# Kernel tuning notes

Measured on AMD Instinct MI355X. Metric: run time of the kernel, lower is better.

The kernel has to match this reference:

```python
import jax, jax.numpy as jnp
import numpy as np

B, M, N, D = 2, 2048, 2048, 2048
N_H, D_H, D_R = 16, 128, 64
THETA = 1000000.0
SCALE = 1.0 / np.sqrt(D_H + D_R)


def build_rope_cache(seq_len, dim, theta):
    freqs = 1.0 / theta ** (jnp.arange(0, dim, 2, dtype=jnp.float32) / dim)
    t = jnp.arange(seq_len, dtype=jnp.float32)
    freqs = jnp.outer(t, freqs)  # (S, dim//2)
    cos = jnp.repeat(jnp.cos(freqs), 2, axis=-1)  # (S, dim)
    sin = jnp.repeat(jnp.sin(freqs), 2, axis=-1)
    return cos, sin


def apply_rope(x, cos, sin):
    # x: (..., S, dim); cos/sin broadcastable (S, dim)
    x_rot = jnp.stack([-x[..., 1::2], x[..., ::2]], axis=-1).reshape(x.shape)
    return x * cos + x_rot * sin


def setup_inputs() -> dict:
    key = jax.random.key(0)
    ks = jax.random.split(key, 8)
    std = 0.02
    return {
        "query": jax.random.normal(ks[0], (B, M, D), jnp.float32),
        "key_value": jax.random.normal(ks[1], (B, N, D), jnp.float32),
        "W_QC": jax.random.normal(ks[2], (N_H * D_H, D), jnp.float32) * std,
        "W_KC": jax.random.normal(ks[3], (N_H * D_H, D), jnp.float32) * std,
        "W_QR": jax.random.normal(ks[4], (N_H * D_R, D), jnp.float32) * std,
        "W_KR": jax.random.normal(ks[5], (N_H * D_R, D), jnp.float32) * std,
        "W_V": jax.random.normal(ks[6], (N_H * D_H, D), jnp.float32) * std,
        "W_O": jax.random.normal(ks[7], (D, N_H * D_H), jnp.float32) * std,
    }


def reference(query, key_value, W_QC, W_KC, W_QR, W_KR, W_V, W_O):
    # projections: torch Linear is x @ W.T
    Q_C = (query @ W_QC.T).reshape(B, M, N_H, D_H).transpose(0, 2, 1, 3)  # (B,H,M,dh)
    K_C = (key_value @ W_KC.T).reshape(B, N, N_H, D_H).transpose(0, 2, 1, 3)
    Q_R = (query @ W_QR.T).reshape(B, M, N_H, D_R).transpose(0, 2, 1, 3)  # (B,H,M,dR)
    K_R = (key_value @ W_KR.T).reshape(B, N, N_H, D_R).transpose(0, 2, 1, 3)
    cos, sin = build_rope_cache(max(M, N), D_R, THETA)
    Q_R = apply_rope(Q_R, cos[:M], sin[:M])
    K_R = apply_rope(K_R, cos[:N], sin[:N])
    scores = (jnp.einsum('bhmd,bhnd->bhmn', Q_C, K_C)
              + jnp.einsum('bhmr,bhnr->bhmn', Q_R, K_R)) * SCALE
    attn = jax.nn.softmax(scores, axis=-1)
    V = (key_value @ W_V.T).reshape(B, N, N_H, D_H).transpose(0, 2, 1, 3)
    out = jnp.einsum('bhmn,bhnd->bhmd', attn, V)  # (B,H,M,dh)
    out = out.transpose(0, 2, 1, 3).reshape(B, M, N_H * D_H)
    return out @ W_O.T
```

## Files before the change

### kernel.cpp

```cpp
#include <hip/hip_runtime.h>
#include <hip/hip_bf16.h>

typedef unsigned short u16;
typedef __attribute__((ext_vector_type(8))) short short8;
typedef __attribute__((ext_vector_type(4))) float floatx4;

#define B_SZ 2
#define M_SZ 2048
#define N_SZ 2048
#define SCALE_F 0.07216878364870323f

__device__ __forceinline__ u16 f2b(float f) {
    unsigned int x = __builtin_bit_cast(unsigned int, f);
    unsigned int r = (x + 0x7fffu + ((x >> 16) & 1u)) >> 16;
    return (u16)r;
}
__device__ __forceinline__ float b2f(u16 u) {
    unsigned int x = ((unsigned int)u) << 16;
    return __builtin_bit_cast(float, x);
}
__device__ __forceinline__ void async16(const void* g, void* l) {
    __builtin_amdgcn_global_load_lds(
        (const __attribute__((address_space(1))) void*)g,
        (__attribute__((address_space(3))) void*)l, 16, 0, 0);
}

__global__ void cast_k(const float* __restrict__ s, u16* __restrict__ d, long n)
{
    const long i = ((long)blockIdx.x * 256 + threadIdx.x) * 4;
    if (i >= n) return;
    const float4 v = *(const float4*)(s + i);
    unsigned long long pk = (unsigned long long)f2b(v.x)
                          | ((unsigned long long)f2b(v.y) << 16)
                          | ((unsigned long long)f2b(v.z) << 32)
                          | ((unsigned long long)f2b(v.w) << 48);
    *(unsigned long long*)(d + i) = pk;
}

__global__ void rope_k(u16* __restrict__ buf)
{
    const int idx = blockIdx.x * 256 + threadIdx.x;
    const int row = idx >> 9;
    const int pr  = idx & 511;
    const int j   = pr & 31;
    const int pos = row & 2047;
    const float f   = powf(1.0e6f, -(float)j * (1.0f / 32.0f));
    const float ang = (float)pos * f;
    float sn, cs;
    sincosf(ang, &sn, &cs);
    u16* pp = buf + ((long)row << 10) + (pr << 1);
    const float x0 = b2f(pp[0]);
    const float x1 = b2f(pp[1]);
    pp[0] = f2b(x0 * cs - x1 * sn);
    pp[1] = f2b(x1 * cs + x0 * sn);
}

template<int MODE>
__global__ void __launch_bounds__(256, 2)
gemm_bt(const u16* __restrict__ A, const u16* __restrict__ Bw,
        void* __restrict__ Cout, int K, int Ndim)
{
    __shared__ u16 As[128 * 64];
    __shared__ u16 Bs[128 * 64];
    const int t = threadIdx.x;
    const int w = t >> 6;
    const int lane = t & 63;
    const int lq = lane >> 4, lr = lane & 15;
    const long tileM = (long)blockIdx.x * 128;
    const long tileN = (long)blockIdx.y * 128;
    const int wm = (w >> 1) * 64, wn = (w & 1) * 64;

    const floatx4 fzero = {0.f, 0.f, 0.f, 0.f};
    floatx4 acc[4][4];
#pragma unroll
    for (int i = 0; i < 4; ++i)
#pragma unroll
        for (int j = 0; j < 4; ++j) acc[i][j] = fzero;

    for (int k0 = 0; k0 < K; k0 += 64) {
#pragma unroll
        for (int r = 0; r < 4; ++r) {
            const int c = r * 256 + t;
            const int row = c >> 3, cc = c & 7;
            const int gcol = ((cc ^ (row & 7)) << 3);
            async16(A + (tileM + row) * (long)K + k0 + gcol, (char*)As + c * 16);
        }
#pragma unroll
        for (int r = 0; r < 4; ++r) {
            const int c = r * 256 + t;
            const int row = c >> 3, cc = c & 7;
            const int gcol = ((cc ^ (row & 7)) << 3);
            async16(Bw + (tileN + row) * (long)K + k0 + gcol, (char*)Bs + c * 16);
        }
        __builtin_amdgcn_s_waitcnt(0);
        __syncthreads();
#pragma unroll
        for (int kk = 0; kk < 2; ++kk) {
            short8 af[4], bfr[4];
#pragma unroll
            for (int i = 0; i < 4; ++i) {
                const int row = wm + 16 * i + lr;
                const int cc = (kk * 4 + lq) ^ (row & 7);
                af[i] = *(const short8*)(As + row * 64 + cc * 8);
            }
#pragma unroll
            for (int j = 0; j < 4; ++j) {
                const int row = wn + 16 * j + lr;
                const int cc = (kk * 4 + lq) ^ (row & 7);
                bfr[j] = *(const short8*)(Bs + row * 64 + cc * 8);
            }
#pragma unroll
            for (int i = 0; i < 4; ++i)
#pragma unroll
                for (int j = 0; j < 4; ++j)
                    acc[i][j] = __builtin_amdgcn_mfma_f32_16x16x32_bf16(
                        af[i], bfr[j], acc[i][j], 0, 0, 0);
        }
        __syncthreads();
    }

#pragma unroll
    for (int i = 0; i < 4; ++i) {
#pragma unroll
        for (int j = 0; j < 4; ++j) {
            const long row0 = tileM + wm + 16 * i + 4 * lq;
            const long col  = tileN + wn + 16 * j + lr;
#pragma unroll
            for (int r = 0; r < 4; ++r) {
                const float v = acc[i][j][r];
                const long row = row0 + r;
                if (MODE == 0) {
                    ((u16*)Cout)[row * Ndim + col] = f2b(v);
                } else if (MODE == 1) {
                    const long b = row >> 11, nn = row & 2047;
                    ((u16*)Cout)[((b * 2048 + col) << 11) + nn] = f2b(v);
                } else {
                    ((float*)Cout)[row * Ndim + col] = v;
                }
            }
        }
    }
}

__global__ void __launch_bounds__(256, 2)
flash_attn(const u16* __restrict__ QC, const u16* __restrict__ QR,
           const u16* __restrict__ KC, const u16* __restrict__ KR,
           const u16* __restrict__ VT, u16* __restrict__ Obuf)
{
    __shared__ u16 KC_s[64 * 128];
    __shared__ u16 KR_s[64 * 64];
    __shared__ u16 VT_s[128 * 64];
    __shared__ u16 P_s[4][32 * 72];

    const int t = threadIdx.x;
    const int w = t >> 6;
    const int lane = t & 63;
    const int lq = lane >> 4, lr = lane & 15;
    const int mb = blockIdx.x;
    const int h  = blockIdx.y;
    const int b  = blockIdx.z;
    const int mbase = mb * 128 + w * 32;

    short8 aq[2][6];
#pragma unroll
    for (int i = 0; i < 2; ++i) {
        const long m = mbase + 16 * i + lr;
        const u16* qc = QC + ((long)b * M_SZ + m) * 2048 + h * 128;
        const u16* qr = QR + ((long)b * M_SZ + m) * 1024 + h * 64;
#pragma unroll
        for (int kc = 0; kc < 4; ++kc) aq[i][kc]     = *(const short8*)(qc + kc * 32 + lq * 8);
#pragma unroll
        for (int kc = 0; kc < 2; ++kc) aq[i][4 + kc] = *(const short8*)(qr + kc * 32 + lq * 8);
    }

    const floatx4 fzero = {0.f, 0.f, 0.f, 0.f};
    float mst[2][4], lst[2][4];
    floatx4 oacc[2][8];
#pragma unroll
    for (int i = 0; i < 2; ++i) {
#pragma unroll
        for (int r = 0; r < 4; ++r) { mst[i][r] = -1e30f; lst[i][r] = 0.f; }
#pragma unroll
        for (int jn = 0; jn < 8; ++jn) oacc[i][jn] = fzero;
    }

    const u16* kc_g = KC + ((long)b * N_SZ) * 2048 + h * 128;
    const u16* kr_g = KR + ((long)b * N_SZ) * 1024 + h * 64;
    const u16* vt_g = VT + ((long)(b * 16 + h) * 128) * 2048;

    for (int kt = 0; kt < 32; ++kt) {
#pragma unroll
        for (int r = 0; r < 4; ++r) {
            const int c = r * 256 + t;
            const int krow = c >> 4, cc = c & 15;
            const int gc = cc ^ (krow & 7);
            async16(kc_g + (long)(kt * 64 + krow) * 2048 + gc * 8, (char*)KC_s + c * 16);
        }
#pragma unroll
        for (int r = 0; r < 2; ++r) {
            const int c = r * 256 + t;
            const int krow = c >> 3, cc = c & 7;
            const int gc = cc ^ (krow & 7);
            async16(kr_g + (long)(kt * 64 + krow) * 1024 + gc * 8, (char*)KR_s + c * 16);
        }
#pragma unroll
        for (int r = 0; r < 4; ++r) {
            const int c = r * 256 + t;
            const int drow = c >> 3, cc = c & 7;
            const int gc = cc ^ (drow & 7);
            async16(vt_g + (long)drow * 2048 + kt * 64 + gc * 8, (char*)VT_s + c * 16);
        }
        __builtin_amdgcn_s_waitcnt(0);
        __syncthreads();

        floatx4 s[2][4];
#pragma unroll
        for (int i = 0; i < 2; ++i)
#pragma unroll
            for (int j = 0; j < 4; ++j) s[i][j] = fzero;
#pragma unroll
        for (int kc = 0; kc < 6; ++kc) {
            short8 bfr[4];
#pragma unroll
            for (int j = 0; j < 4; ++j) {
                const int krow = 16 * j + lr;
                if (kc < 4) {
                    const int cc = (4 * kc + lq) ^ (krow & 7);
                    bfr[j] = *(const short8*)(KC_s + krow * 128 + cc * 8);
                } else {
                    const int cc = (4 * (kc - 4) + lq) ^ (krow & 7);
                    bfr[j] = *(const short8*)(KR_s + krow * 64 + cc * 8);
                }
            }
#pragma unroll
            for (int i = 0; i < 2; ++i)
#pragma unroll
                for (int j = 0; j < 4; ++j)
                    s[i][j] = __builtin_amdgcn_mfma_f32_16x16x32_bf16(
                        aq[i][kc], bfr[j], s[i][j], 0, 0, 0);
        }

#pragma unroll
        for (int i = 0; i < 2; ++i) {
            float rmax[4], rsum[4], alpha[4];
#pragma unroll
            for (int j = 0; j < 4; ++j)
#pragma unroll
                for (int r = 0; r < 4; ++r) s[i][j][r] *= SCALE_F;
#pragma unroll
            for (int r = 0; r < 4; ++r)
                rmax[r] = fmaxf(fmaxf(s[i][0][r], s[i][1][r]), fmaxf(s[i][2][r], s[i][3][r]));
#pragma unroll
            for (int d = 1; d < 16; d <<= 1)
#pragma unroll
                for (int r = 0; r < 4; ++r)
                    rmax[r] = fmaxf(rmax[r], __shfl_xor(rmax[r], d, 64));
#pragma unroll
            for (int r = 0; r < 4; ++r) {
                const float mnew = fmaxf(mst[i][r], rmax[r]);
                alpha[r] = __expf(mst[i][r] - mnew);
                mst[i][r] = mnew;
                rsum[r] = 0.f;
            }
#pragma unroll
            for (int j = 0; j < 4; ++j)
#pragma unroll
                for (int r = 0; r < 4; ++r) {
                    const float p = __expf(s[i][j][r] - mst[i][r]);
                    s[i][j][r] = p;
                    rsum[r] += p;
                }
#pragma unroll
            for (int d = 1; d < 16; d <<= 1)
#pragma unroll
                for (int r = 0; r < 4; ++r)
                    rsum[r] += __shfl_xor(rsum[r], d, 64);
#pragma unroll
            for (int r = 0; r < 4; ++r)
                lst[i][r] = lst[i][r] * alpha[r] + rsum[r];
#pragma unroll
            for (int jn = 0; jn < 8; ++jn)
#pragma unroll
                for (int r = 0; r < 4; ++r) oacc[i][jn][r] *= alpha[r];
            u16* pw = &P_s[w][0];
#pragma unroll
            for (int j = 0; j < 4; ++j)
#pragma unroll
                for (int r = 0; r < 4; ++r)
                    pw[(16 * i + 4 * lq + r) * 72 + 16 * j + lr] = f2b(s[i][j][r]);
        }

#pragma unroll
        for (int kc = 0; kc < 2; ++kc) {
            short8 ap[2];
#pragma unroll
            for (int i = 0; i < 2; ++i)
                ap[i] = *(const short8*)(&P_s[w][0] + (16 * i + lr) * 72 + kc * 32 + lq * 8);
#pragma unroll
            for (int jn = 0; jn < 8; ++jn) {
                const int drow = 16 * jn + lr;
                const int cc = (4 * kc + lq) ^ (drow & 7);
                const short8 bv = *(const short8*)(VT_s + drow * 64 + cc * 8);
#pragma unroll
                for (int i = 0; i < 2; ++i)
                    oacc[i][jn] = __builtin_amdgcn_mfma_f32_16x16x32_bf16(
                        ap[i], bv, oacc[i][jn], 0, 0, 0);
            }
        }
        __syncthreads();
    }

#pragma unroll
    for (int i = 0; i < 2; ++i)
#pragma unroll
        for (int jn = 0; jn < 8; ++jn)
#pragma unroll
            for (int r = 0; r < 4; ++r) {
                const long row = mbase + 16 * i + 4 * lq + r;
                const int d = 16 * jn + lr;
                const float v = oacc[i][jn][r] / lst[i][r];
                Obuf[((long)b * M_SZ + row) * 2048 + h * 128 + d] = f2b(v);
            }
}

extern "C" void kernel_launch(void* const* d_in, const int* in_sizes, int n_in,
                              void* d_out, int out_size, void* d_ws, size_t ws_size,
                              hipStream_t stream)
{
    (void)in_sizes; (void)n_in; (void)out_size; (void)ws_size;
    const float* q   = (const float*)d_in[0];
    const float* kv  = (const float*)d_in[1];
    const float* wqc = (const float*)d_in[2];
    const float* wkc = (const float*)d_in[3];
    const float* wqr = (const float*)d_in[4];
    const float* wkr = (const float*)d_in[5];
    const float* wv  = (const float*)d_in[6];
    const float* wo  = (const float*)d_in[7];

    u16* p = (u16*)d_ws;
    u16* qbf  = p; p += 8388608;
    u16* kvbf = p; p += 8388608;
    u16* wqcb = p; p += 4194304;
    u16* wkcb = p; p += 4194304;
    u16* wqrb = p; p += 2097152;
    u16* wkrb = p; p += 2097152;
    u16* wvb  = p; p += 4194304;
    u16* wob  = p; p += 4194304;
    u16* QCb  = p; p += 8388608;
    u16* KCb  = p; p += 8388608;
    u16* QRb  = p; p += 4194304;
    u16* KRb  = p; p += 4194304;
    u16* VTb  = p; p += 8388608;
    u16* Ob   = p; p += 8388608;

    cast_k<<<8192, 256, 0, stream>>>(q,   qbf,  8388608);
    cast_k<<<8192, 256, 0, stream>>>(kv,  kvbf, 8388608);
    cast_k<<<4096, 256, 0, stream>>>(wqc, wqcb, 4194304);
    cast_k<<<4096, 256, 0, stream>>>(wkc, wkcb, 4194304);
    cast_k<<<2048, 256, 0, stream>>>(wqr, wqrb, 2097152);
    cast_k<<<2048, 256, 0, stream>>>(wkr, wkrb, 2097152);
    cast_k<<<4096, 256, 0, stream>>>(wv,  wvb,  4194304);
    cast_k<<<4096, 256, 0, stream>>>(wo,  wob,  4194304);

    dim3 g1(32, 16), g2(32, 8);
    gemm_bt<0><<<g1, 256, 0, stream>>>(qbf,  wqcb, QCb, 2048, 2048);
    gemm_bt<0><<<g1, 256, 0, stream>>>(kvbf, wkcb, KCb, 2048, 2048);
    gemm_bt<0><<<g2, 256, 0, stream>>>(qbf,  wqrb, QRb, 2048, 1024);
    gemm_bt<0><<<g2, 256, 0, stream>>>(kvbf, wkrb, KRb, 2048, 1024);
    gemm_bt<1><<<g1, 256, 0, stream>>>(kvbf, wvb,  VTb, 2048, 2048);

    rope_k<<<8192, 256, 0, stream>>>(QRb);
    rope_k<<<8192, 256, 0, stream>>>(KRb);

    dim3 gf(16, 16, 2);
    flash_attn<<<gf, 256, 0, stream>>>(QCb, QRb, KCb, KRb, VTb, Ob);

    gemm_bt<2><<<g1, 256, 0, stream>>>(Ob, wob, d_out, 2048, 2048);
}
```

Measured before the change: 585.3 us.

## Fuse casts, concatenate projection weights, fuse RoPE into GEMM epilogue, streamline softmax

Replaces the eight cast launches with a single multi-segment cast kernel that also folds the softmax scale and log2(e) into the query. Projection weights are concatenated so Q and KV projections each run as one GEMM, and RoPE and V-transpose are applied in the GEMM epilogue, which removes the separate rope kernels and their memory round-trips. The flash-attention softmax switches to exp2, skips the rescale when no row max increases, and packs P conversions. GEMM launch bounds are raised to 3 blocks per SM, which may constrain registers. Folding the scale into bf16 query rounding slightly changes numerics.

Measured after the change: 513.9 us. -12.2%, faster.

```diff
diff --git a/kernel.cpp b/kernel.cpp
--- a/kernel.cpp
+++ b/kernel.cpp
@@ -2,22 +2,27 @@
 #include <hip/hip_bf16.h>
 
 typedef unsigned short u16;
+typedef unsigned int u32;
+typedef unsigned long long u64;
 typedef __attribute__((ext_vector_type(8))) short short8;
 typedef __attribute__((ext_vector_type(4))) float floatx4;
 
-#define B_SZ 2
-#define M_SZ 2048
-#define N_SZ 2048
-#define SCALE_F 0.07216878364870323f
+#if __has_builtin(__builtin_amdgcn_exp2f)
+#define EXP2F(x) __builtin_amdgcn_exp2f(x)
+#else
+#define EXP2F(x) exp2f(x)
+#endif
+
+#define QSCALE (0.07216878364870323f * 1.4426950408889634f)
+#define ROPE_C 0.62286151779f
 
 __device__ __forceinline__ u16 f2b(float f) {
     unsigned int x = __builtin_bit_cast(unsigned int, f);
     unsigned int r = (x + 0x7fffu + ((x >> 16) & 1u)) >> 16;
     return (u16)r;
 }
-__device__ __forceinline__ float b2f(u16 u) {
-    unsigned int x = ((unsigned int)u) << 16;
-    return __builtin_bit_cast(float, x);
+__device__ __forceinline__ u32 pk2(float a, float b) {
+    return (u32)f2b(a) | ((u32)f2b(b) << 16);
 }
 __device__ __forceinline__ void async16(const void* g, void* l) {
     __builtin_amdgcn_global_load_lds(
@@ -25,40 +30,32 @@
         (__attribute__((address_space(3))) void*)l, 16, 0, 0);
 }
 
-__global__ void cast_k(const float* __restrict__ s, u16* __restrict__ d, long n)
+struct CastArgs {
+    const float* src[8];
+    u16* dst[8];
+    float scale[8];
+    int startblk[8];
+};
+
+__global__ void cast_all_k(CastArgs a)
 {
-    const long i = ((long)blockIdx.x * 256 + threadIdx.x) * 4;
-    if (i >= n) return;
-    const float4 v = *(const float4*)(s + i);
-    unsigned long long pk = (unsigned long long)f2b(v.x)
-                          | ((unsigned long long)f2b(v.y) << 16)
-                          | ((unsigned long long)f2b(v.z) << 32)
-                          | ((unsigned long long)f2b(v.w) << 48);
-    *(unsigned long long*)(d + i) = pk;
-}
-
-__global__ void rope_k(u16* __restrict__ buf)
-{
-    const int idx = blockIdx.x * 256 + threadIdx.x;
-    const int row = idx >> 9;
-    const int pr  = idx & 511;
-    const int j   = pr & 31;
-    const int pos = row & 2047;
-    const float f   = powf(1.0e6f, -(float)j * (1.0f / 32.0f));
-    const float ang = (float)pos * f;
-    float sn, cs;
-    sincosf(ang, &sn, &cs);
-    u16* pp = buf + ((long)row << 10) + (pr << 1);
-    const float x0 = b2f(pp[0]);
-    const float x1 = b2f(pp[1]);
-    pp[0] = f2b(x0 * cs - x1 * sn);
-    pp[1] = f2b(x1 * cs + x0 * sn);
-}
-
-template<int MODE>
-__global__ void __launch_bounds__(256, 2)
+    const int bid = blockIdx.x;
+    int s = 0;
+#pragma unroll
+    for (int i = 1; i < 8; ++i) s += (bid >= a.startblk[i]);
+    const long idx = ((long)(bid - a.startblk[s]) * 256 + threadIdx.x) * 4;
+    const float4 v = *(const float4*)(a.src[s] + idx);
+    const float sc = a.scale[s];
+    const u64 pk = (u64)pk2(v.x * sc, v.y * sc)
+                 | ((u64)pk2(v.z * sc, v.w * sc) << 32);
+    *(u64*)(a.dst[s] + idx) = pk;
+}
+
+template<int EPI>
+__global__ void __launch_bounds__(256, 3)
 gemm_bt(const u16* __restrict__ A, const u16* __restrict__ Bw,
-        void* __restrict__ Cout, int K, int Ndim)
+        void* __restrict__ out0, u16* __restrict__ out1, u16* __restrict__ out2,
+        int K)
 {
     __shared__ u16 As[128 * 64];
     __shared__ u16 Bs[128 * 64];
@@ -119,24 +116,42 @@
         __syncthreads();
     }
 
+    const bool isV    = (EPI == 1) && (tileN >= 3072);
+    const bool isRope = (EPI != 2) && !isV && (tileN >= 2048);
+
 #pragma unroll
     for (int i = 0; i < 4; ++i) {
 #pragma unroll
         for (int j = 0; j < 4; ++j) {
             const long row0 = tileM + wm + 16 * i + 4 * lq;
             const long col  = tileN + wn + 16 * j + lr;
-#pragma unroll
-            for (int r = 0; r < 4; ++r) {
-                const float v = acc[i][j][r];
-                const long row = row0 + r;
-                if (MODE == 0) {
-                    ((u16*)Cout)[row * Ndim + col] = f2b(v);
-                } else if (MODE == 1) {
-                    const long b = row >> 11, nn = row & 2047;
-                    ((u16*)Cout)[((b * 2048 + col) << 11) + nn] = f2b(v);
-                } else {
-                    ((float*)Cout)[row * Ndim + col] = v;
+            if (EPI == 2) {
+#pragma unroll
+                for (int r = 0; r < 4; ++r)
+                    ((float*)out0)[(row0 + r) * 2048 + col] = acc[i][j][r];
+            } else if (isV) {
+                const u32 lo = pk2(acc[i][j][0], acc[i][j][1]);
+                const u32 hi = pk2(acc[i][j][2], acc[i][j][3]);
+                const long bb = row0 >> 11;
+                u16* dst = out2 + ((bb * 2048 + (col - 3072)) << 11) + (row0 & 2047);
+                *(uint2*)dst = make_uint2(lo, hi);
+            } else if (isRope) {
+                const int jj = ((int)col & 63) >> 1;
+                const float freq = EXP2F(-ROPE_C * (float)jj);
+#pragma unroll
+                for (int r = 0; r < 4; ++r) {
+                    const float v = acc[i][j][r];
+                    const float vp = __shfl_xor(v, 1, 64);
+                    const long row = row0 + r;
+                    float sn, cs;
+                    __sincosf((float)(row & 2047) * freq, &sn, &cs);
+                    const float o = (col & 1) ? (v * cs + vp * sn) : (v * cs - vp * sn);
+                    out1[row * 1024 + (col - 2048)] = f2b(o);
                 }
+            } else {
+#pragma unroll
+                for (int r = 0; r < 4; ++r)
+                    ((u16*)out0)[(row0 + r) * 2048 + col] = f2b(acc[i][j][r]);
             }
         }
     }
@@ -156,17 +171,15 @@
     const int w = t >> 6;
     const int lane = t & 63;
     const int lq = lane >> 4, lr = lane & 15;
-    const int mb = blockIdx.x;
-    const int h  = blockIdx.y;
-    const int b  = blockIdx.z;
-    const int mbase = mb * 128 + w * 32;
+    const int mbase = blockIdx.x * 128 + w * 32;
+    const int h = blockIdx.y, b = blockIdx.z;
 
     short8 aq[2][6];
 #pragma unroll
     for (int i = 0; i < 2; ++i) {
         const long m = mbase + 16 * i + lr;
-        const u16* qc = QC + ((long)b * M_SZ + m) * 2048 + h * 128;
-        const u16* qr = QR + ((long)b * M_SZ + m) * 1024 + h * 64;
+        const u16* qc = QC + ((long)b * 2048 + m) * 2048 + h * 128;
+        const u16* qr = QR + ((long)b * 2048 + m) * 1024 + h * 64;
 #pragma unroll
         for (int kc = 0; kc < 4; ++kc) aq[i][kc]     = *(const short8*)(qc + kc * 32 + lq * 8);
 #pragma unroll
@@ -184,8 +197,8 @@
         for (int jn = 0; jn < 8; ++jn) oacc[i][jn] = fzero;
     }
 
-    const u16* kc_g = KC + ((long)b * N_SZ) * 2048 + h * 128;
-    const u16* kr_g = KR + ((long)b * N_SZ) * 1024 + h * 64;
+    const u16* kc_g = KC + ((long)b * 2048) * 2048 + h * 128;
+    const u16* kr_g = KR + ((long)b * 2048) * 1024 + h * 64;
     const u16* vt_g = VT + ((long)(b * 16 + h) * 128) * 2048;
 
     for (int kt = 0; kt < 32; ++kt) {
@@ -240,55 +253,85 @@
                         aq[i][kc], bfr[j], s[i][j], 0, 0, 0);
         }
 
-#pragma unroll
-        for (int i = 0; i < 2; ++i) {
-            float rmax[4], rsum[4], alpha[4];
+        float rmax[2][4];
+#pragma unroll
+        for (int i = 0; i < 2; ++i)
+#pragma unroll
+            for (int r = 0; r < 4; ++r)
+                rmax[i][r] = fmaxf(fmaxf(s[i][0][r], s[i][1][r]),
+                                   fmaxf(s[i][2][r], s[i][3][r]));
+#pragma unroll
+        for (int d = 1; d < 16; d <<= 1)
+#pragma unroll
+            for (int i = 0; i < 2; ++i)
+#pragma unroll
+                for (int r = 0; r < 4; ++r)
+                    rmax[i][r] = fmaxf(rmax[i][r], __shfl_xor(rmax[i][r], d, 64));
+
+        int upd = 0;
+#pragma unroll
+        for (int i = 0; i < 2; ++i)
+#pragma unroll
+            for (int r = 0; r < 4; ++r) upd |= (rmax[i][r] > mst[i][r]);
+
+        if (__any(upd)) {
+#pragma unroll
+            for (int i = 0; i < 2; ++i) {
+                float alpha[4];
+#pragma unroll
+                for (int r = 0; r < 4; ++r) {
+                    const float mnew = fmaxf(mst[i][r], rmax[i][r]);
+                    alpha[r] = EXP2F(mst[i][r] - mnew);
+                    mst[i][r] = mnew;
+                    lst[i][r] *= alpha[r];
+                }
+#pragma unroll
+                for (int jn = 0; jn < 8; ++jn)
+#pragma unroll
+                    for (int r = 0; r < 4; ++r) oacc[i][jn][r] *= alpha[r];
+            }
+        }
+
+        float rsum[2][4];
+#pragma unroll
+        for (int i = 0; i < 2; ++i)
+#pragma unroll
+            for (int r = 0; r < 4; ++r) rsum[i][r] = 0.f;
+#pragma unroll
+        for (int i = 0; i < 2; ++i)
 #pragma unroll
             for (int j = 0; j < 4; ++j)
 #pragma unroll
-                for (int r = 0; r < 4; ++r) s[i][j][r] *= SCALE_F;
-#pragma unroll
-            for (int r = 0; r < 4; ++r)
-                rmax[r] = fmaxf(fmaxf(s[i][0][r], s[i][1][r]), fmaxf(s[i][2][r], s[i][3][r]));
-#pragma unroll
-            for (int d = 1; d < 16; d <<= 1)
+                for (int r = 0; r < 4; ++r) {
+                    const float p = EXP2F(s[i][j][r] - mst[i][r]);
+                    s[i][j][r] = p;
+                    rsum[i][r] += p;
+                }
+#pragma unroll
+        for (int d = 1; d < 16; d <<= 1)
+#pragma unroll
+            for (int i = 0; i < 2; ++i)
 #pragma unroll
                 for (int r = 0; r < 4; ++r)
-                    rmax[r] = fmaxf(rmax[r], __shfl_xor(rmax[r], d, 64));
-#pragma unroll
-            for (int r = 0; r < 4; ++r) {
-                const float mnew = fmaxf(mst[i][r], rmax[r]);
-                alpha[r] = __expf(mst[i][r] - mnew);
-                mst[i][r] = mnew;
-                rsum[r] = 0.f;
-            }
-#pragma unroll
-            for (int j = 0; j < 4; ++j)
-#pragma unroll
-                for (int r = 0; r < 4; ++r) {
-                    const float p = __expf(s[i][j][r] - mst[i][r]);
-                    s[i][j][r] = p;
-                    rsum[r] += p;
-                }
-#pragma unroll
-            for (int d = 1; d < 16; d <<= 1)
-#pragma unroll
-                for (int r = 0; r < 4; ++r)
-                    rsum[r] += __shfl_xor(rsum[r], d, 64);
-#pragma unroll
-            for (int r = 0; r < 4; ++r)
-                lst[i][r] = lst[i][r] * alpha[r] + rsum[r];
-#pragma unroll
-            for (int jn = 0; jn < 8; ++jn)
-#pragma unroll
-                for (int r = 0; r < 4; ++r) oacc[i][jn][r] *= alpha[r];
-            u16* pw = &P_s[w][0];
-#pragma unroll
-            for (int j = 0; j < 4; ++j)
-#pragma unroll
-                for (int r = 0; r < 4; ++r)
-                    pw[(16 * i + 4 * lq + r) * 72 + 16 * j + lr] = f2b(s[i][j][r]);
-        }
+                    rsum[i][r] += __shfl_xor(rsum[i][r], d, 64);
+#pragma unroll
+        for (int i = 0; i < 2; ++i)
+#pragma unroll
+            for (int r = 0; r < 4; ++r) lst[i][r] += rsum[i][r];
+
+        u16* pw = &P_s[w][0];
+#pragma unroll
+        for (int i = 0; i < 2; ++i)
+#pragma unroll
+            for (int j = 0; j < 4; ++j) {
+                const u32 d0 = pk2(s[i][j][0], s[i][j][1]);
+                const u32 d1 = pk2(s[i][j][2], s[i][j][3]);
+                const int base = (16 * i + 4 * lq) * 72 + 16 * j + lr;
+                pw[base]       = (u16)d0;
+                pw[base + 72]  = (u16)(d0 >> 16);
+                pw[base + 144] = (u16)d1;
+                pw[base + 216] = (u16)(d1 >> 16);
+            }
 
 #pragma unroll
         for (int kc = 0; kc < 2; ++kc) {
@@ -319,7 +362,7 @@
                 const long row = mbase + 16 * i + 4 * lq + r;
                 const int d = 16 * jn + lr;
                 const float v = oacc[i][jn][r] / lst[i][r];
-                Obuf[((long)b * M_SZ + row) * 2048 + h * 128 + d] = f2b(v);
+                Obuf[((long)b * 2048 + row) * 2048 + h * 128 + d] = f2b(v);
             }
 }
 
@@ -328,52 +371,39 @@
                               hipStream_t stream)
 {
     (void)in_sizes; (void)n_in; (void)out_size; (void)ws_size;
-    const float* q   = (const float*)d_in[0];
-    const float* kv  = (const float*)d_in[1];
-    const float* wqc = (const float*)d_in[2];
-    const float* wkc = (const float*)d_in[3];
-    const float* wqr = (const float*)d_in[4];
-    const float* wkr = (const float*)d_in[5];
-    const float* wv  = (const float*)d_in[6];
-    const float* wo  = (const float*)d_in[7];
 
     u16* p = (u16*)d_ws;
-    u16* qbf  = p; p += 8388608;
-    u16* kvbf = p; p += 8388608;
-    u16* wqcb = p; p += 4194304;
-    u16* wkcb = p; p += 4194304;
-    u16* wqrb = p; p += 2097152;
-    u16* wkrb = p; p += 2097152;
-    u16* wvb  = p; p += 4194304;
-    u16* wob  = p; p += 4194304;
-    u16* QCb  = p; p += 8388608;
-    u16* KCb  = p; p += 8388608;
-    u16* QRb  = p; p += 4194304;
-    u16* KRb  = p; p += 4194304;
-    u16* VTb  = p; p += 8388608;
-    u16* Ob   = p; p += 8388608;
-
-    cast_k<<<8192, 256, 0, stream>>>(q,   qbf,  8388608);
-    cast_k<<<8192, 256, 0, stream>>>(kv,  kvbf, 8388608);
-    cast_k<<<4096, 256, 0, stream>>>(wqc, wqcb, 4194304);
-    cast_k<<<4096, 256, 0, stream>>>(wkc, wkcb, 4194304);
-    cast_k<<<2048, 256, 0, stream>>>(wqr, wqrb, 2097152);
-    cast_k<<<2048, 256, 0, stream>>>(wkr, wkrb, 2097152);
-    cast_k<<<4096, 256, 0, stream>>>(wv,  wvb,  4194304);
-    cast_k<<<4096, 256, 0, stream>>>(wo,  wob,  4194304);
-
-    dim3 g1(32, 16), g2(32, 8);
-    gemm_bt<0><<<g1, 256, 0, stream>>>(qbf,  wqcb, QCb, 2048, 2048);
-    gemm_bt<0><<<g1, 256, 0, stream>>>(kvbf, wkcb, KCb, 2048, 2048);
-    gemm_bt<0><<<g2, 256, 0, stream>>>(qbf,  wqrb, QRb, 2048, 1024);
-    gemm_bt<0><<<g2, 256, 0, stream>>>(kvbf, wkrb, KRb, 2048, 1024);
-    gemm_bt<1><<<g1, 256, 0, stream>>>(kvbf, wvb,  VTb, 2048, 2048);
-
-    rope_k<<<8192, 256, 0, stream>>>(QRb);
-    rope_k<<<8192, 256, 0, stream>>>(KRb);
-
-    dim3 gf(16, 16, 2);
-    flash_attn<<<gf, 256, 0, stream>>>(QCb, QRb, KCb, KRb, VTb, Ob);
-
-    gemm_bt<2><<<g1, 256, 0, stream>>>(Ob, wob, d_out, 2048, 2048);
-}
+    u16* qbf   = p; p += 8388608;
+    u16* kvbf  = p; p += 8388608;
+    u16* wqall = p; p += 6291456;
+    u16* wkvall= p; p += 10485760;
+    u16* wob   = p; p += 4194304;
+    u16* QCb   = p; p += 8388608;
+    u16* QRb   = p; p += 4194304;
+    u16* KCb   = p; p += 8388608;
+    u16* KRb   = p; p += 4194304;
+    u16* VTb   = p; p += 8388608;
+    u16* Ob    = p; p += 8388608;
+
+    CastArgs a;
+    a.src[0] = (const float*)d_in[0]; a.dst[0] = qbf;               a.scale[0] = QSCALE;
+    a.src[1] = (const float*)d_in[1]; a.dst[1] = kvbf;              a.scale[1] = 1.f;
+    a.src[2] = (const float*)d_in[2]; a.dst[2] = wqall;             a.scale[2] = 1.f;
+    a.src[3] = (const float*)d_in[3]; a.dst[3] = wkvall;            a.scale[3] = 1.f;
+    a.src[4] = (const float*)d_in[4]; a.dst[4] = wqall + 4194304;   a.scale[4] = 1.f;
+    a.src[5] = (const float*)d_in[5]; a.dst[5] = wkvall + 4194304;  a.scale[5] = 1.f;
+    a.src[6] = (const float*)d_in[6]; a.dst[6] = wkvall + 6291456;  a.scale[6] = 1.f;
+    a.src[7] = (const float*)d_in[7]; a.dst[7] = wob;               a.scale[7] = 1.f;
+    const int blks[8] = {8192, 8192, 4096, 4096, 2048, 2048, 4096, 4096};
+    int acc = 0;
+    for (int i = 0; i < 8; ++i) { a.startblk[i] = acc; acc += blks[i]; }
+
+    cast_all_k<<<acc, 256, 0, stream>>>(a);
+
+    gemm_bt<0><<<dim3(32, 24), 256, 0, stream>>>(qbf,  wqall,  QCb, QRb, nullptr, 2048);
+    gemm_bt<1><<<dim3(32, 40), 256, 0, stream>>>(kvbf, wkvall, KCb, KRb, VTb,     2048);
+
+    flash_attn<<<dim3(16, 16, 2), 256, 0, stream>>>(QCb, QRb, KCb, KRb, VTb, Ob);
+
+    gemm_bt<2><<<dim3(32, 16), 256, 0, stream>>>(Ob, wob, d_out, nullptr, nullptr, 2048);
+}
```
